# Kernel tuning notes

Hardware: AMD Instinct MI355X
Metric: run time of the kernel (lower is better)

## Reference

```python
import jax, jax.numpy as jnp
import numpy as np

N = 100000
E = 1600000
F = 128
C = 10
G = 256  # number of graphs in the batch
K = 2    # num_layers


def setup_inputs() -> dict:
    key = jax.random.key(0)
    k1, k2, k3, k4, k5 = jax.random.split(key, 5)
    x = jax.random.normal(k1, (N, F), dtype=jnp.float32)
    edge_index = jax.random.randint(k2, (2, E), 0, N, dtype=jnp.int64)
    batch = jnp.sort(jax.random.randint(k3, (N,), 0, G, dtype=jnp.int64))
    W = jax.random.normal(k4, (F, C), dtype=jnp.float32) * (1.0 / np.sqrt(F))
    b = jax.random.normal(k5, (C,), dtype=jnp.float32) * 0.01
    return {"x": x, "edge_index": edge_index, "batch": batch, "W": W, "b": b}


def reference(x, edge_index, batch, W, b):
    row, col = edge_index[0], edge_index[1]
    # K rounds of unweighted adjacency SpMM: out[i] = sum_{(i,j) in E} x[j]
    h = x
    for _ in range(K):
        h = jax.ops.segment_sum(h[col], row, num_segments=N)  # [N, F]
    # mean pooling per graph
    sums = jax.ops.segment_sum(h, batch, num_segments=G)  # [G, F]
    counts = jax.ops.segment_sum(jnp.ones((N,), dtype=h.dtype), batch, num_segments=G)
    pooled = sums / jnp.maximum(counts, 1.0)[:, None]
    # final linear classifier
    return pooled @ W + b  # [G, C]
```

## Files before the change

kernel.cpp:

```cpp
#include <hip/hip_runtime.h>
#include <hip/hip_fp16.h>

#define NN 100000
#define EE 1600000
#define FF 128
#define CC 10
#define GG 256
#define PC 16
#define WSH 7
#define NW 782
#define WCAP 2560
#define EPB 8192
#define PB 196
#define XB 391


__global__ __launch_bounds__(1024) void prep(
        const int* __restrict__ eidx, int* __restrict__ wfill,
        unsigned int* __restrict__ rec,
        const float4* __restrict__ x4, const float* __restrict__ W,
        uint2* __restrict__ y0, int E, int N) {
    __shared__ alignas(16) union {
        struct {
            unsigned int srec[EPB];
            unsigned short sw[EPB];
            int lcnt[NW];
            int lofs[NW];
            int lcur[NW];
            int lgb[NW];
            int sscan[1024];
        } p;
        float wt[CC * FF];
    } u;

    const int tid = threadIdx.x;

    if (blockIdx.x < PB) {
        const int e0 = blockIdx.x * EPB;
        const int n = min(EPB, E - e0);

        for (int i = tid; i < NW; i += 1024) u.p.lcnt[i] = 0;
        __syncthreads();

        int rr[8], cc[8];
        #pragma unroll
        for (int k = 0; k < 8; ++k) {
            int i = tid + (k << 10);
            if (i < n) {
                rr[k] = eidx[e0 + i];
                cc[k] = eidx[EE + e0 + i];
                atomicAdd(&u.p.lcnt[rr[k] >> WSH], 1);
            }
        }
        __syncthreads();

        u.p.sscan[tid] = (tid < NW) ? u.p.lcnt[tid] : 0;
        __syncthreads();
        for (int s = 1; s < 1024; s <<= 1) {
            int t = 0;
            if (tid >= s) t = u.p.sscan[tid - s];
            __syncthreads();
            if (tid >= s) u.p.sscan[tid] += t;
            __syncthreads();
        }
        if (tid < NW) {
            int excl = u.p.sscan[tid] - u.p.lcnt[tid];
            u.p.lofs[tid] = excl;
            u.p.lcur[tid] = excl;
        }
        __syncthreads();

        #pragma unroll
        for (int k = 0; k < 8; ++k) {
            int i = tid + (k << 10);
            if (i < n) {
                int w = rr[k] >> WSH;
                int p = atomicAdd(&u.p.lcur[w], 1);
                u.p.srec[p] = ((unsigned int)(rr[k] & 127) << 17) | (unsigned int)cc[k];
                u.p.sw[p] = (unsigned short)w;
            }
        }
        __syncthreads();

        if (tid < NW) {
            int cw = u.p.lcnt[tid];
            u.p.lgb[tid] = cw ? atomicAdd(&wfill[tid], cw) : 0;
        }
        __syncthreads();

        for (int i = tid; i < n; i += 1024) {
            int w = u.p.sw[i];
            int pos = u.p.lgb[w] + (i - u.p.lofs[w]);
            if (pos < WCAP) rec[(size_t)w * WCAP + pos] = u.p.srec[i];
        }
    } else {
        float4* WT = (float4*)u.wt;
        for (int i = tid; i < CC * 32; i += 1024) {
            int c = i >> 5, k = i & 31;
            WT[i >> 5 == c ? c * 32 + k : 0] = make_float4(
                W[(4 * k + 0) * CC + c], W[(4 * k + 1) * CC + c],
                W[(4 * k + 2) * CC + c], W[(4 * k + 3) * CC + c]);
        }
        __syncthreads();
        int node = (blockIdx.x - PB) * 256 + (tid >> 2);
        int lane = tid & 3;
        if (node >= N) return;
        float a[CC];
        #pragma unroll
        for (int c = 0; c < CC; ++c) a[c] = 0.f;
        #pragma unroll
        for (int k = 0; k < 8; ++k) {
            float4 xv = x4[(size_t)node * 32 + k * 4 + lane];
            #pragma unroll
            for (int c = 0; c < CC; ++c) {
                float4 wv = WT[c * 32 + k * 4 + lane];
                a[c] += xv.x * wv.x + xv.y * wv.y + xv.z * wv.z + xv.w * wv.w;
            }
        }
        #pragma unroll
        for (int c = 0; c < CC; ++c) {
            a[c] += __shfl_xor(a[c], 1);
            a[c] += __shfl_xor(a[c], 2);
        }
        float4 o;
        if (lane == 0)      o = make_float4(a[0], a[1], a[2], a[3]);
        else if (lane == 1) o = make_float4(a[4], a[5], a[6], a[7]);
        else if (lane == 2) o = make_float4(a[8], a[9], 0.f, 0.f);
        else                o = make_float4(0.f, 0.f, 0.f, 0.f);
        __half2 h01 = __floats2half2_rn(o.x, o.y);
        __half2 h23 = __floats2half2_rn(o.z, o.w);
        uint2 pkd;
        pkd.x = *(unsigned int*)&h01;
        pkd.y = *(unsigned int*)&h23;
        y0[(size_t)node * 4 + lane] = pkd;
    }
}

__device__ __forceinline__ void acc_half4(float4& acc, uint2 v) {
    __half2 h0 = *(__half2*)&v.x;
    __half2 h1 = *(__half2*)&v.y;
    float2 f0 = __half22float2(h0);
    float2 f1 = __half22float2(h1);
    acc.x += f0.x; acc.y += f0.y; acc.z += f1.x; acc.w += f1.y;
}


template<bool POOL>
__global__ __launch_bounds__(512) void window_spmm(
        const uint2* __restrict__ src,
        const unsigned int* __restrict__ rec,
        const int* __restrict__ wfill, const int* __restrict__ batch,
        uint2* __restrict__ dst, float* __restrict__ pooled,
        int* __restrict__ gcount, int N) {
    __shared__ int cnt[128];
    __shared__ int sscan[128];
    __shared__ int rptr[129];
    __shared__ int cur[128];
    __shared__ int lcols[WCAP];
    __shared__ float spool[32 * PC];
    __shared__ int spcnt[32];
    __shared__ int sbatch[128];

    const int tid = threadIdx.x;
    const int w = blockIdx.x;
    const int row0 = w << WSH;
    const int n = min(wfill[w], WCAP);
    const unsigned int* rp = rec + (size_t)w * WCAP;

    if (tid < 128) {
        cnt[tid] = 0;
        if (POOL) {
            int node = row0 + tid;
            sbatch[tid] = (node < N) ? batch[node] : -1;
        }
    }
    if (POOL) {
        for (int i = tid; i < 32 * PC; i += 512) spool[i] = 0.f;
        if (tid < 32) spcnt[tid] = 0;
    }
    __syncthreads();

    for (int i = tid; i < n; i += 512)
        atomicAdd(&cnt[rp[i] >> 17], 1);
    __syncthreads();

    if (tid < 128) sscan[tid] = cnt[tid];
    __syncthreads();
    for (int s = 1; s < 128; s <<= 1) {
        int t = 0;
        if (tid < 128 && tid >= s) t = sscan[tid - s];
        __syncthreads();
        if (tid < 128 && tid >= s) sscan[tid] += t;
        __syncthreads();
    }
    if (tid < 128) {
        int excl = sscan[tid] - cnt[tid];
        rptr[tid] = excl;
        cur[tid] = excl;
        if (tid == 127) rptr[128] = sscan[127];
    }
    __syncthreads();

    for (int i = tid; i < n; i += 512) {
        unsigned int rcv = rp[i];
        int p = atomicAdd(&cur[rcv >> 17], 1);
        lcols[p] = (int)(rcv & 0x1FFFF);
    }
    __syncthreads();

    const int q = tid >> 2;
    const int lane = tid & 3;
    const int node = row0 + q;
    float4 acc = make_float4(0.f, 0.f, 0.f, 0.f);
    float4 acc2 = make_float4(0.f, 0.f, 0.f, 0.f);
    int e = rptr[q];
    const int e1 = rptr[q + 1];
    for (; e + 4 <= e1; e += 4) {
        int c0 = lcols[e], c1 = lcols[e + 1], c2 = lcols[e + 2], c3 = lcols[e + 3];
        uint2 v0 = src[(size_t)c0 * 4 + lane];
        uint2 v1 = src[(size_t)c1 * 4 + lane];
        uint2 v2 = src[(size_t)c2 * 4 + lane];
        uint2 v3 = src[(size_t)c3 * 4 + lane];
        acc_half4(acc, v0);
        acc_half4(acc2, v1);
        acc_half4(acc, v2);
        acc_half4(acc2, v3);
    }
    for (; e < e1; ++e) {
        uint2 v = src[(size_t)lcols[e] * 4 + lane];
        acc_half4(acc, v);
    }
    acc.x += acc2.x; acc.y += acc2.y; acc.z += acc2.z; acc.w += acc2.w;

    if (!POOL) {
        if (node < N) {
            __half2 h01 = __floats2half2_rn(acc.x, acc.y);
            __half2 h23 = __floats2half2_rn(acc.z, acc.w);
            uint2 pkd;
            pkd.x = *(unsigned int*)&h01;
            pkd.y = *(unsigned int*)&h23;
            dst[(size_t)node * 4 + lane] = pkd;
        }
    } else {
        int g_first = sbatch[0];
        if (node < N) {
            int g = sbatch[q];
            int idx = g - g_first;
            if (idx < 32) {
                float* sp = &spool[idx * PC + lane * 4];
                atomicAdd(sp + 0, acc.x);
                atomicAdd(sp + 1, acc.y);
                atomicAdd(sp + 2, acc.z);
                atomicAdd(sp + 3, acc.w);
                if (lane == 0) atomicAdd(&spcnt[idx], 1);
            } else {
                float* pp = pooled + (size_t)g * PC + lane * 4;
                unsafeAtomicAdd(pp + 0, acc.x);
                unsafeAtomicAdd(pp + 1, acc.y);
                unsafeAtomicAdd(pp + 2, acc.z);
                unsafeAtomicAdd(pp + 3, acc.w);
                if (lane == 0) atomicAdd(&gcount[g], 1);
            }
        }
        __syncthreads();
        int lastrl = min(row0 + 127, N - 1) - row0;
        int span = min(sbatch[lastrl] - g_first + 1, 32);
        for (int t = tid; t < span * PC; t += 512) {
            float v = spool[t];
            if (v != 0.f)
                unsafeAtomicAdd(&pooled[(size_t)(g_first + (t >> 4)) * PC + (t & 15)], v);
        }
        if (tid < span && spcnt[tid] > 0)
            atomicAdd(&gcount[g_first + tid], spcnt[tid]);
    }
}


__global__ void finalize(const float* __restrict__ pooled, const int* __restrict__ gcount,
                         const float* __restrict__ bvec, float* __restrict__ out) {
    int idx = blockIdx.x * blockDim.x + threadIdx.x;
    if (idx >= GG * CC) return;
    int g = idx / CC, c = idx % CC;
    int cg = gcount[g];
    out[idx] = pooled[g * PC + c] / (float)(cg > 0 ? cg : 1) + bvec[c];
}


static inline size_t al256(size_t x) { return (x + 255) & ~(size_t)255; }

extern "C" void kernel_launch(void* const* d_in, const int* in_sizes, int n_in,
                              void* d_out, int out_size, void* d_ws, size_t ws_size,
                              hipStream_t stream) {
    const float* x    = (const float*)d_in[0];
    const int*   eidx = (const int*)d_in[1];
    const int*   batch= (const int*)d_in[2];
    const float* W    = (const float*)d_in[3];
    const float* bvec = (const float*)d_in[4];
    float* out = (float*)d_out;

    char* p = (char*)d_ws;
    float* pooled = (float*)p; p += al256((size_t)GG * PC * 4);
    int*   wfill  = (int*)p;   p += al256((size_t)NW * 4);
    int*   gcount = (int*)p;   p += al256((size_t)GG * 4);
    size_t zbytes = (size_t)(p - (char*)d_ws);
    unsigned int* rec = (unsigned int*)p; p += al256((size_t)NW * WCAP * 4);
    uint2* y0     = (uint2*)p; p += al256((size_t)NW * 128 * 32);
    uint2* y1     = (uint2*)p; p += al256((size_t)NW * 128 * 32);

    hipMemsetAsync(d_ws, 0, zbytes, stream);

    prep<<<PB + XB, 1024, 0, stream>>>(eidx, wfill, rec,
                                       (const float4*)x, W, y0, EE, NN);

    window_spmm<false><<<NW, 512, 0, stream>>>(y0, rec, wfill, nullptr,
                                               y1, nullptr, nullptr, NN);

    window_spmm<true><<<NW, 512, 0, stream>>>(y1, rec, wfill, batch,
                                              nullptr, pooled, gcount, NN);

    finalize<<<(GG * CC + 255) / 256, 256, 0, stream>>>(pooled, gcount, bvec, out);
}
```

Measured before the change: 73.49 us.

## Register-cache window records, unroll gather 8-wide, zero pool buffers in prep

```diff
diff --git a/kernel.cpp b/kernel.cpp
--- a/kernel.cpp
+++ b/kernel.cpp
@@ -19,7 +19,8 @@
         const int* __restrict__ eidx, int* __restrict__ wfill,
         unsigned int* __restrict__ rec,
         const float4* __restrict__ x4, const float* __restrict__ W,
-        uint2* __restrict__ y0, int E, int N) {
+        uint2* __restrict__ y0, float* __restrict__ pooled,
+        int* __restrict__ gcount, int E, int N) {
     __shared__ alignas(16) union {
         struct {
             unsigned int srec[EPB];
@@ -94,10 +95,14 @@
             if (pos < WCAP) rec[(size_t)w * WCAP + pos] = u.p.srec[i];
         }
     } else {
+        if (blockIdx.x == PB) {
+            for (int i = tid; i < GG * PC; i += 1024) pooled[i] = 0.f;
+            if (tid < GG) gcount[tid] = 0;
+        }
         float4* WT = (float4*)u.wt;
         for (int i = tid; i < CC * 32; i += 1024) {
             int c = i >> 5, k = i & 31;
-            WT[i >> 5 == c ? c * 32 + k : 0] = make_float4(
+            WT[c * 32 + k] = make_float4(
                 W[(4 * k + 0) * CC + c], W[(4 * k + 1) * CC + c],
                 W[(4 * k + 2) * CC + c], W[(4 * k + 3) * CC + c]);
         }
@@ -180,8 +185,19 @@
     }
     __syncthreads();
 
-    for (int i = tid; i < n; i += 512)
-        atomicAdd(&cnt[rp[i] >> 17], 1);
+    const int i1 = tid + 512, i2 = tid + 1024, i3 = tid + 1536, i4 = tid + 2048;
+    unsigned int r0 = 0, r1 = 0, r2 = 0, r3 = 0, r4 = 0;
+    if (tid < n) r0 = rp[tid];
+    if (i1 < n) r1 = rp[i1];
+    if (i2 < n) r2 = rp[i2];
+    if (i3 < n) r3 = rp[i3];
+    if (i4 < n) r4 = rp[i4];
+
+    if (tid < n) atomicAdd(&cnt[r0 >> 17], 1);
+    if (i1 < n) atomicAdd(&cnt[r1 >> 17], 1);
+    if (i2 < n) atomicAdd(&cnt[r2 >> 17], 1);
+    if (i3 < n) atomicAdd(&cnt[r3 >> 17], 1);
+    if (i4 < n) atomicAdd(&cnt[r4 >> 17], 1);
     __syncthreads();
 
     if (tid < 128) sscan[tid] = cnt[tid];
@@ -201,11 +217,11 @@
     }
     __syncthreads();
 
-    for (int i = tid; i < n; i += 512) {
-        unsigned int rcv = rp[i];
-        int p = atomicAdd(&cur[rcv >> 17], 1);
-        lcols[p] = (int)(rcv & 0x1FFFF);
-    }
+    if (tid < n) { int p = atomicAdd(&cur[r0 >> 17], 1); lcols[p] = (int)(r0 & 0x1FFFF); }
+    if (i1 < n) { int p = atomicAdd(&cur[r1 >> 17], 1); lcols[p] = (int)(r1 & 0x1FFFF); }
+    if (i2 < n) { int p = atomicAdd(&cur[r2 >> 17], 1); lcols[p] = (int)(r2 & 0x1FFFF); }
+    if (i3 < n) { int p = atomicAdd(&cur[r3 >> 17], 1); lcols[p] = (int)(r3 & 0x1FFFF); }
+    if (i4 < n) { int p = atomicAdd(&cur[r4 >> 17], 1); lcols[p] = (int)(r4 & 0x1FFFF); }
     __syncthreads();
 
     const int q = tid >> 2;
@@ -213,24 +229,44 @@
     const int node = row0 + q;
     float4 acc = make_float4(0.f, 0.f, 0.f, 0.f);
     float4 acc2 = make_float4(0.f, 0.f, 0.f, 0.f);
+    float4 acc3 = make_float4(0.f, 0.f, 0.f, 0.f);
+    float4 acc4 = make_float4(0.f, 0.f, 0.f, 0.f);
     int e = rptr[q];
     const int e1 = rptr[q + 1];
-    for (; e + 4 <= e1; e += 4) {
-        int c0 = lcols[e], c1 = lcols[e + 1], c2 = lcols[e + 2], c3 = lcols[e + 3];
+    for (; e + 8 <= e1; e += 8) {
+        int c0 = lcols[e],     c1 = lcols[e + 1], c2 = lcols[e + 2], c3 = lcols[e + 3];
+        int c4 = lcols[e + 4], c5 = lcols[e + 5], c6 = lcols[e + 6], c7 = lcols[e + 7];
         uint2 v0 = src[(size_t)c0 * 4 + lane];
         uint2 v1 = src[(size_t)c1 * 4 + lane];
         uint2 v2 = src[(size_t)c2 * 4 + lane];
         uint2 v3 = src[(size_t)c3 * 4 + lane];
+        uint2 v4 = src[(size_t)c4 * 4 + lane];
+        uint2 v5 = src[(size_t)c5 * 4 + lane];
+        uint2 v6 = src[(size_t)c6 * 4 + lane];
+        uint2 v7 = src[(size_t)c7 * 4 + lane];
         acc_half4(acc, v0);
         acc_half4(acc2, v1);
-        acc_half4(acc, v2);
-        acc_half4(acc2, v3);
-    }
-    for (; e < e1; ++e) {
+        acc_half4(acc3, v2);
+        acc_half4(acc4, v3);
+        acc_half4(acc, v4);
+        acc_half4(acc2, v5);
+        acc_half4(acc3, v6);
+        acc_half4(acc4, v7);
+    }
+    for (; e + 2 <= e1; e += 2) {
+        int c0 = lcols[e], c1 = lcols[e + 1];
+        uint2 v0 = src[(size_t)c0 * 4 + lane];
+        uint2 v1 = src[(size_t)c1 * 4 + lane];
+        acc_half4(acc, v0);
+        acc_half4(acc2, v1);
+    }
+    if (e < e1) {
         uint2 v = src[(size_t)lcols[e] * 4 + lane];
         acc_half4(acc, v);
     }
     acc.x += acc2.x; acc.y += acc2.y; acc.z += acc2.z; acc.w += acc2.w;
+    acc3.x += acc4.x; acc3.y += acc4.y; acc3.z += acc4.z; acc3.w += acc4.w;
+    acc.x += acc3.x; acc.y += acc3.y; acc.z += acc3.z; acc.w += acc3.w;
 
     if (!POOL) {
         if (node < N) {
@@ -299,18 +335,18 @@
     float* out = (float*)d_out;
 
     char* p = (char*)d_ws;
+    int*   wfill  = (int*)p;   p += al256((size_t)NW * 4);
+    size_t zbytes = (size_t)(p - (char*)d_ws);
     float* pooled = (float*)p; p += al256((size_t)GG * PC * 4);
-    int*   wfill  = (int*)p;   p += al256((size_t)NW * 4);
     int*   gcount = (int*)p;   p += al256((size_t)GG * 4);
-    size_t zbytes = (size_t)(p - (char*)d_ws);
     unsigned int* rec = (unsigned int*)p; p += al256((size_t)NW * WCAP * 4);
     uint2* y0     = (uint2*)p; p += al256((size_t)NW * 128 * 32);
     uint2* y1     = (uint2*)p; p += al256((size_t)NW * 128 * 32);
 
-    hipMemsetAsync(d_ws, 0, zbytes, stream);
+    hipMemsetAsync(wfill, 0, zbytes, stream);
 
     prep<<<PB + XB, 1024, 0, stream>>>(eidx, wfill, rec,
-                                       (const float4*)x, W, y0, EE, NN);
+                                       (const float4*)x, W, y0, pooled, gcount, EE, NN);
 
     window_spmm<false><<<NW, 512, 0, stream>>>(y0, rec, wfill, nullptr,
                                                y1, nullptr, nullptr, NN);
```

Result: faster. 70.18 us, median of 2 (-4.5%).
